# Performance work log

Hardware: AMD Instinct MI355X
Metric: run time of the kernel (lower is better)

The kernel has to match this reference:

```python
import jax, jax.numpy as jnp
import numpy as np

B, T, D, L, E = 4096, 4, 1024, 2, 4  # batch, tasks (risk_num+1), dim, layers, experts/task


def setup_inputs() -> dict:
    key = jax.random.key(0)
    ks = jax.random.split(key, 9)
    s = 1.0 / np.sqrt(D).astype(np.float32)  # torch Linear-style uniform scale
    se = 1.0 / np.sqrt(E).astype(np.float32)
    u = lambda k, shape, sc: jax.random.uniform(k, shape, jnp.float32, -sc, sc)
    return {
        "x": jax.random.normal(ks[0], (B, T, D), jnp.float32),
        # per-layer, per-task shared-expert MLP params (mlp_level=2)
        "W1": u(ks[1], (L, T, D, D), s), "b1": u(ks[2], (L, T, D), s),
        "W2": u(ks[3], (L, T, D, D), s), "b2": u(ks[4], (L, T, D), s),
        # integration weights over E (aliased) experts per task
        "inte": u(ks[5], (L, T, E), se),
        # one shared gate per layer: Linear(D -> T) + softmax
        "Wg": u(ks[6], (L, D, T), s), "bg": u(ks[7], (L, T), s),
    }


def reference(x, W1, b1, W2, b2, inte, Wg, bg):
    h = x  # [B, T, D]
    n_layers = W1.shape[0]
    for l in range(n_layers):
        # per-task 2-layer MLP expert (all E experts per task share weights in the
        # original due to [MLP]*E aliasing)
        t1 = jax.nn.relu(jnp.einsum('btd,tdo->bto', h, W1[l]) + b1[l])
        t2 = jax.nn.relu(jnp.einsum('btd,tdo->bto', t1, W2[l]) + b2[l])
        # stack of E identical expert outputs einsum'd with inte weights == scale by sum_e w[t,e]
        teo = t2 * jnp.sum(inte[l], axis=-1)[None, :, None]  # [B, T, D]
        # shared gate applied to each task's output: softmax(Linear(teo)) -> [B, T, T]
        g = jax.nn.softmax(jnp.einsum('btd,dk->btk', teo, Wg[l]) + bg[l], axis=-1)
        # bmm combine + residual
        h = jnp.einsum('btk,bkd->btd', g, teo) + teo
    return h
```

## Files before the change

kernel.cpp:

```cpp
#include <hip/hip_runtime.h>
#include <hip/hip_bf16.h>

#define B_ 4096
#define T_ 4
#define D_ 1024
#define E_ 4

typedef unsigned short ushort_t;
typedef float f32x4 __attribute__((ext_vector_type(4)));
typedef short bf16x8 __attribute__((ext_vector_type(8)));

__device__ __forceinline__ unsigned short f2bf(float f) {
    unsigned int u = __float_as_uint(f);
    u += 0x7FFF + ((u >> 16) & 1);
    return (unsigned short)(u >> 16);
}

#define GLOBAL_LOAD_LDS16(gp, lp)                                                        \
    __builtin_amdgcn_global_load_lds((const __attribute__((address_space(1))) void*)(gp),\
                                     (__attribute__((address_space(3))) void*)(lp),      \
                                     16, 0, 0)

__global__ __launch_bounds__(256) void k_convert_x(const float* __restrict__ x,
                                                   ushort_t* __restrict__ hbf) {
    int idx = (blockIdx.x * 256 + threadIdx.x) * 4;
    int d = idx & (D_ - 1);
    int t = (idx >> 10) & 3;
    int b = idx >> 12;
    const float4 v = *(const float4*)(x + idx);
    ushort4 o = { f2bf(v.x), f2bf(v.y), f2bf(v.z), f2bf(v.w) };
    *(ushort4*)(hbf + (size_t)t * B_ * D_ + (size_t)b * D_ + d) = o;
}

__global__ __launch_bounds__(256) void k_transpose_w(const float* __restrict__ W1,
                                                     const float* __restrict__ W2,
                                                     ushort_t* __restrict__ W1t,
                                                     ushort_t* __restrict__ W2t) {
    __shared__ float tile[32][33];
    const int z = blockIdx.z;
    const float* src = (z < 8) ? (W1 + (size_t)z * D_ * D_) : (W2 + (size_t)(z - 8) * D_ * D_);
    ushort_t* dst = (z < 8) ? (W1t + (size_t)z * D_ * D_) : (W2t + (size_t)(z - 8) * D_ * D_);
    const int o0 = blockIdx.x * 32, d0 = blockIdx.y * 32;
    const int tx = threadIdx.x, ty = threadIdx.y;
#pragma unroll
    for (int j = 0; j < 4; ++j)
        tile[ty + 8 * j][tx] = src[(size_t)(d0 + ty + 8 * j) * D_ + o0 + tx];
    __syncthreads();
#pragma unroll
    for (int j = 0; j < 4; ++j)
        dst[(size_t)(o0 + ty + 8 * j) * D_ + d0 + tx] = f2bf(tile[tx][ty + 8 * j]);
}

template <bool OUT_BF16>
__global__ __launch_bounds__(512, 4) void k_gemm_bt(
    const ushort_t* __restrict__ A,
    const ushort_t* __restrict__ Bt,
    const float* __restrict__ bias,
    void* __restrict__ out,
    const float* __restrict__ inte)
{
    const int f = blockIdx.x;
    const int xcd = f & 7;
    const int t = xcd >> 1;
    const int m_blk = ((f >> 6) << 1) | (xcd & 1);
    const int n_blk = (f >> 3) & 7;
    const int m0 = m_blk * 256, n0 = n_blk * 128;

    const ushort_t* Ap = A + (size_t)t * B_ * D_;
    const ushort_t* Bp = Bt + (size_t)t * D_ * D_;
    const float* bp = bias + t * D_;

    __shared__ __align__(16) ushort_t As[2][256 * 32];
    __shared__ __align__(16) ushort_t Bs[2][128 * 32];

    const int tid = threadIdx.x;
    const int lane = tid & 63, wid = tid >> 6;
    const int lr = lane & 15, quad = lane >> 4;
    const int wm = (wid & 3) * 64, wn = (wid >> 2) * 64;

    f32x4 acc[4][4] = {};

    const int qa0 = wid * 64 + lane;
    const int qa1 = qa0 + 512;
    const int qb  = qa0;
    const ushort_t* ga0 = Ap + (size_t)(m0 + (qa0 >> 2)) * D_ + (qa0 & 3) * 8;
    const ushort_t* ga1 = Ap + (size_t)(m0 + (qa1 >> 2)) * D_ + (qa1 & 3) * 8;
    const ushort_t* gb  = Bp + (size_t)(n0 + (qb  >> 2)) * D_ + (qb  & 3) * 8;

#define STAGE(k0, s)                                              \
    do {                                                          \
        GLOBAL_LOAD_LDS16(ga0 + (k0), As[s] + wid * 512);         \
        GLOBAL_LOAD_LDS16(ga1 + (k0), As[s] + 4096 + wid * 512);  \
        GLOBAL_LOAD_LDS16(gb  + (k0), Bs[s] + wid * 512);         \
    } while (0)

    STAGE(0, 0);
    int s = 0;
    for (int k0 = 0; k0 < D_; k0 += 32, s ^= 1) {
        __syncthreads();
        if (k0 + 32 < D_) STAGE(k0 + 32, s ^ 1);
        bf16x8 af[4], bfv[4];
#pragma unroll
        for (int mi = 0; mi < 4; ++mi)
            af[mi] = *(const bf16x8*)(As[s] + (wm + mi * 16 + lr) * 32 + quad * 8);
#pragma unroll
        for (int ni = 0; ni < 4; ++ni)
            bfv[ni] = *(const bf16x8*)(Bs[s] + (wn + ni * 16 + lr) * 32 + quad * 8);
#pragma unroll
        for (int mi = 0; mi < 4; ++mi)
#pragma unroll
            for (int ni = 0; ni < 4; ++ni)
                acc[mi][ni] = __builtin_amdgcn_mfma_f32_16x16x32_bf16(
                    af[mi], bfv[ni], acc[mi][ni], 0, 0, 0);
    }
#undef STAGE

    float scale = 1.0f;
    if (inte) {
        const float* ip = inte + t * E_;
        scale = ip[0] + ip[1] + ip[2] + ip[3];
    }
#pragma unroll
    for (int mi = 0; mi < 4; ++mi) {
#pragma unroll
        for (int ni = 0; ni < 4; ++ni) {
            const int gcol = n0 + wn + ni * 16 + lr;
            const float bv = bp[gcol];
#pragma unroll
            for (int r = 0; r < 4; ++r) {
                const int grow = m0 + wm + mi * 16 + quad * 4 + r;
                float v = acc[mi][ni][r] + bv;
                v = fmaxf(v, 0.0f) * scale;
                const size_t off = (size_t)t * B_ * D_ + (size_t)grow * D_ + gcol;
                if (OUT_BF16) ((ushort_t*)out)[off] = f2bf(v);
                else          ((float*)out)[off] = v;
            }
        }
    }
}

template <bool FINAL>
__global__ __launch_bounds__(256) void k_gate_combine(
    const float* __restrict__ teo,
    const float* __restrict__ Wg,
    const float* __restrict__ bg,
    void* __restrict__ out)
{
    const int b = blockIdx.x;
    const int tid = threadIdx.x;
    const int d0 = tid * 4;

    float4 tv[4];
#pragma unroll
    for (int t = 0; t < 4; ++t)
        tv[t] = *(const float4*)(teo + (size_t)t * B_ * D_ + (size_t)b * D_ + d0);
    float4 wg[4];
#pragma unroll
    for (int i = 0; i < 4; ++i)
        wg[i] = *(const float4*)(Wg + (size_t)(d0 + i) * 4);

    float p[16];
#pragma unroll
    for (int t = 0; t < 4; ++t) {
        const float* tvp = (const float*)&tv[t];
#pragma unroll
        for (int k = 0; k < 4; ++k) {
            p[t * 4 + k] = tvp[0] * ((const float*)&wg[0])[k]
                         + tvp[1] * ((const float*)&wg[1])[k]
                         + tvp[2] * ((const float*)&wg[2])[k]
                         + tvp[3] * ((const float*)&wg[3])[k];
        }
    }
#pragma unroll
    for (int i = 0; i < 16; ++i) {
        float v = p[i];
        v += __shfl_xor(v, 1, 64);
        v += __shfl_xor(v, 2, 64);
        v += __shfl_xor(v, 4, 64);
        v += __shfl_xor(v, 8, 64);
        p[i] = v;
    }
    __shared__ float red[16][16];
    __shared__ float fin[16];
    const int grp = tid >> 4;
    if ((tid & 15) == 0) {
#pragma unroll
        for (int i = 0; i < 16; ++i) red[grp][i] = p[i];
    }
    __syncthreads();
    if (tid < 16) {
        float v = 0.0f;
#pragma unroll
        for (int g = 0; g < 16; ++g) v += red[g][tid];
        fin[tid] = v;
    }
    __syncthreads();

    float g[4][4];
#pragma unroll
    for (int t = 0; t < 4; ++t) {
        float lg[4];
#pragma unroll
        for (int k = 0; k < 4; ++k)
            lg[k] = fin[t * 4 + k] + bg[k];
        float mx = fmaxf(fmaxf(lg[0], lg[1]), fmaxf(lg[2], lg[3]));
        float e0 = __expf(lg[0] - mx), e1 = __expf(lg[1] - mx);
        float e2 = __expf(lg[2] - mx), e3 = __expf(lg[3] - mx);
        float inv = 1.0f / (e0 + e1 + e2 + e3);
        g[t][0] = e0 * inv; g[t][1] = e1 * inv; g[t][2] = e2 * inv; g[t][3] = e3 * inv;
    }
#pragma unroll
    for (int t = 0; t < 4; ++t) {
        float o[4];
#pragma unroll
        for (int i = 0; i < 4; ++i) {
            o[i] = g[t][0] * ((const float*)&tv[0])[i]
                 + g[t][1] * ((const float*)&tv[1])[i]
                 + g[t][2] * ((const float*)&tv[2])[i]
                 + g[t][3] * ((const float*)&tv[3])[i]
                 + ((const float*)&tv[t])[i];
        }
        if (FINAL) {
            float4 ov = { o[0], o[1], o[2], o[3] };
            *(float4*)((float*)out + (size_t)b * T_ * D_ + (size_t)t * D_ + d0) = ov;
        } else {
            ushort4 ov = { f2bf(o[0]), f2bf(o[1]), f2bf(o[2]), f2bf(o[3]) };
            *(ushort4*)((ushort_t*)out + (size_t)t * B_ * D_ + (size_t)b * D_ + d0) = ov;
        }
    }
}

extern "C" void kernel_launch(void* const* d_in, const int* in_sizes, int n_in,
                              void* d_out, int out_size, void* d_ws, size_t ws_size,
                              hipStream_t stream) {
    const float* x    = (const float*)d_in[0];
    const float* W1   = (const float*)d_in[1];
    const float* b1   = (const float*)d_in[2];
    const float* W2   = (const float*)d_in[3];
    const float* b2   = (const float*)d_in[4];
    const float* inte = (const float*)d_in[5];
    const float* Wg   = (const float*)d_in[6];
    const float* bg   = (const float*)d_in[7];

    char* ws = (char*)d_ws;
    ushort_t* W1t  = (ushort_t*)(ws);
    ushort_t* W2t  = (ushort_t*)(ws + 33554432);
    ushort_t* Hbf  = (ushort_t*)(ws + 67108864);
    ushort_t* T1bf = (ushort_t*)(ws + 100663296);
    float*    Teo  = (float*)   (ws + 134217728);

    k_convert_x<<<dim3(B_ * T_ * D_ / 1024), 256, 0, stream>>>(x, Hbf);
    k_transpose_w<<<dim3(D_ / 32, D_ / 32, 16), dim3(32, 8), 0, stream>>>(W1, W2, W1t, W2t);

    for (int l = 0; l < 2; ++l) {
        const size_t wOff = (size_t)l * T_ * D_ * D_;
        k_gemm_bt<true ><<<dim3(512), 512, 0, stream>>>(Hbf, W1t + wOff, b1 + l * T_ * D_,
                                                        (void*)T1bf, nullptr);
        k_gemm_bt<false><<<dim3(512), 512, 0, stream>>>(T1bf, W2t + wOff, b2 + l * T_ * D_,
                                                        (void*)Teo, inte + l * T_ * E_);
        if (l == 0)
            k_gate_combine<false><<<dim3(B_), 256, 0, stream>>>(
                Teo, Wg + l * D_ * T_, bg + l * T_, (void*)Hbf);
        else
            k_gate_combine<true ><<<dim3(B_), 256, 0, stream>>>(
                Teo, Wg + l * D_ * T_, bg + l * T_, (void*)d_out);
    }
}
```

Measured before the change: 377.9 us.

## Use 32x32 MFMA with swizzled LDS, merge prep kernels, bf16 layer-0 teo

```diff
diff --git a/kernel.cpp b/kernel.cpp
--- a/kernel.cpp
+++ b/kernel.cpp
@@ -7,7 +7,7 @@
 #define E_ 4
 
 typedef unsigned short ushort_t;
-typedef float f32x4 __attribute__((ext_vector_type(4)));
+typedef float f32x16 __attribute__((ext_vector_type(16)));
 typedef short bf16x8 __attribute__((ext_vector_type(8)));
 
 __device__ __forceinline__ unsigned short f2bf(float f) {
@@ -15,33 +15,42 @@
     u += 0x7FFF + ((u >> 16) & 1);
     return (unsigned short)(u >> 16);
 }
+__device__ __forceinline__ float bf2f(unsigned short u) {
+    return __uint_as_float(((unsigned int)u) << 16);
+}
 
 #define GLOBAL_LOAD_LDS16(gp, lp)                                                        \
     __builtin_amdgcn_global_load_lds((const __attribute__((address_space(1))) void*)(gp),\
                                      (__attribute__((address_space(3))) void*)(lp),      \
                                      16, 0, 0)
 
-__global__ __launch_bounds__(256) void k_convert_x(const float* __restrict__ x,
-                                                   ushort_t* __restrict__ hbf) {
-    int idx = (blockIdx.x * 256 + threadIdx.x) * 4;
-    int d = idx & (D_ - 1);
-    int t = (idx >> 10) & 3;
-    int b = idx >> 12;
-    const float4 v = *(const float4*)(x + idx);
-    ushort4 o = { f2bf(v.x), f2bf(v.y), f2bf(v.z), f2bf(v.w) };
-    *(ushort4*)(hbf + (size_t)t * B_ * D_ + (size_t)b * D_ + d) = o;
-}
-
-__global__ __launch_bounds__(256) void k_transpose_w(const float* __restrict__ W1,
-                                                     const float* __restrict__ W2,
-                                                     ushort_t* __restrict__ W1t,
-                                                     ushort_t* __restrict__ W2t) {
+#define LSLOT_E(row, kq) (((((row) << 2) + ((kq) ^ (((row) >> 1) & 3)))) << 3)
+#define KQOF(q) ((((q) & 3) ^ (((q) >> 3) & 3)) * 8)
+
+__global__ __launch_bounds__(256) void k_prep(const float* __restrict__ x,
+                                              const float* __restrict__ W1,
+                                              const float* __restrict__ W2,
+                                              ushort_t* __restrict__ hbf,
+                                              ushort_t* __restrict__ W1t,
+                                              ushort_t* __restrict__ W2t) {
+    const int z = blockIdx.z;
+    const int tid = threadIdx.x;
+    if (z >= 16) {
+        const int blk = (z - 16) * 1024 + blockIdx.y * 32 + blockIdx.x;
+        const int idx = (blk * 256 + tid) * 4;
+        const int d = idx & (D_ - 1);
+        const int t = (idx >> 10) & 3;
+        const int b = idx >> 12;
+        const float4 v = *(const float4*)(x + idx);
+        ushort4 o = { f2bf(v.x), f2bf(v.y), f2bf(v.z), f2bf(v.w) };
+        *(ushort4*)(hbf + (size_t)t * B_ * D_ + (size_t)b * D_ + d) = o;
+        return;
+    }
     __shared__ float tile[32][33];
-    const int z = blockIdx.z;
     const float* src = (z < 8) ? (W1 + (size_t)z * D_ * D_) : (W2 + (size_t)(z - 8) * D_ * D_);
     ushort_t* dst = (z < 8) ? (W1t + (size_t)z * D_ * D_) : (W2t + (size_t)(z - 8) * D_ * D_);
     const int o0 = blockIdx.x * 32, d0 = blockIdx.y * 32;
-    const int tx = threadIdx.x, ty = threadIdx.y;
+    const int tx = tid & 31, ty = tid >> 5;
 #pragma unroll
     for (int j = 0; j < 4; ++j)
         tile[ty + 8 * j][tx] = src[(size_t)(d0 + ty + 8 * j) * D_ + o0 + tx];
@@ -75,17 +84,17 @@
 
     const int tid = threadIdx.x;
     const int lane = tid & 63, wid = tid >> 6;
-    const int lr = lane & 15, quad = lane >> 4;
+    const int l31 = lane & 31, lh = lane >> 5;
     const int wm = (wid & 3) * 64, wn = (wid >> 2) * 64;
 
-    f32x4 acc[4][4] = {};
+    f32x16 acc[2][2] = {};
 
     const int qa0 = wid * 64 + lane;
     const int qa1 = qa0 + 512;
     const int qb  = qa0;
-    const ushort_t* ga0 = Ap + (size_t)(m0 + (qa0 >> 2)) * D_ + (qa0 & 3) * 8;
-    const ushort_t* ga1 = Ap + (size_t)(m0 + (qa1 >> 2)) * D_ + (qa1 & 3) * 8;
-    const ushort_t* gb  = Bp + (size_t)(n0 + (qb  >> 2)) * D_ + (qb  & 3) * 8;
+    const ushort_t* ga0 = Ap + (size_t)(m0 + (qa0 >> 2)) * D_ + KQOF(qa0);
+    const ushort_t* ga1 = Ap + (size_t)(m0 + (qa1 >> 2)) * D_ + KQOF(qa1);
+    const ushort_t* gb  = Bp + (size_t)(n0 + (qb  >> 2)) * D_ + KQOF(qb);
 
 #define STAGE(k0, s)                                              \
     do {                                                          \
@@ -99,19 +108,25 @@
     for (int k0 = 0; k0 < D_; k0 += 32, s ^= 1) {
         __syncthreads();
         if (k0 + 32 < D_) STAGE(k0 + 32, s ^ 1);
-        bf16x8 af[4], bfv[4];
-#pragma unroll
-        for (int mi = 0; mi < 4; ++mi)
-            af[mi] = *(const bf16x8*)(As[s] + (wm + mi * 16 + lr) * 32 + quad * 8);
-#pragma unroll
-        for (int ni = 0; ni < 4; ++ni)
-            bfv[ni] = *(const bf16x8*)(Bs[s] + (wn + ni * 16 + lr) * 32 + quad * 8);
-#pragma unroll
-        for (int mi = 0; mi < 4; ++mi)
-#pragma unroll
-            for (int ni = 0; ni < 4; ++ni)
-                acc[mi][ni] = __builtin_amdgcn_mfma_f32_16x16x32_bf16(
-                    af[mi], bfv[ni], acc[mi][ni], 0, 0, 0);
+        bf16x8 af[2][2], bfv[2][2];
+#pragma unroll
+        for (int mi = 0; mi < 2; ++mi)
+#pragma unroll
+            for (int ks = 0; ks < 2; ++ks)
+                af[mi][ks] = *(const bf16x8*)(As[s] + LSLOT_E(wm + mi * 32 + l31, ks * 2 + lh));
+#pragma unroll
+        for (int ni = 0; ni < 2; ++ni)
+#pragma unroll
+            for (int ks = 0; ks < 2; ++ks)
+                bfv[ni][ks] = *(const bf16x8*)(Bs[s] + LSLOT_E(wn + ni * 32 + l31, ks * 2 + lh));
+#pragma unroll
+        for (int ks = 0; ks < 2; ++ks)
+#pragma unroll
+            for (int mi = 0; mi < 2; ++mi)
+#pragma unroll
+                for (int ni = 0; ni < 2; ++ni)
+                    acc[mi][ni] = __builtin_amdgcn_mfma_f32_32x32x16_bf16(
+                        af[mi][ks], bfv[ni][ks], acc[mi][ni], 0, 0, 0);
     }
 #undef STAGE
 
@@ -121,15 +136,15 @@
         scale = ip[0] + ip[1] + ip[2] + ip[3];
     }
 #pragma unroll
-    for (int mi = 0; mi < 4; ++mi) {
-#pragma unroll
-        for (int ni = 0; ni < 4; ++ni) {
-            const int gcol = n0 + wn + ni * 16 + lr;
+    for (int mi = 0; mi < 2; ++mi) {
+#pragma unroll
+        for (int ni = 0; ni < 2; ++ni) {
+            const int gcol = n0 + wn + ni * 32 + l31;
             const float bv = bp[gcol];
 #pragma unroll
-            for (int r = 0; r < 4; ++r) {
-                const int grow = m0 + wm + mi * 16 + quad * 4 + r;
-                float v = acc[mi][ni][r] + bv;
+            for (int reg = 0; reg < 16; ++reg) {
+                const int grow = m0 + wm + mi * 32 + (reg & 3) + 8 * (reg >> 2) + 4 * lh;
+                float v = acc[mi][ni][reg] + bv;
                 v = fmaxf(v, 0.0f) * scale;
                 const size_t off = (size_t)t * B_ * D_ + (size_t)grow * D_ + gcol;
                 if (OUT_BF16) ((ushort_t*)out)[off] = f2bf(v);
@@ -139,9 +154,9 @@
     }
 }
 
-template <bool FINAL>
+template <bool FINAL, bool TEO_BF16>
 __global__ __launch_bounds__(256) void k_gate_combine(
-    const float* __restrict__ teo,
+    const void* __restrict__ teo_v,
     const float* __restrict__ Wg,
     const float* __restrict__ bg,
     void* __restrict__ out)
@@ -152,8 +167,16 @@
 
     float4 tv[4];
 #pragma unroll
-    for (int t = 0; t < 4; ++t)
-        tv[t] = *(const float4*)(teo + (size_t)t * B_ * D_ + (size_t)b * D_ + d0);
+    for (int t = 0; t < 4; ++t) {
+        if (TEO_BF16) {
+            const ushort4 u = *(const ushort4*)((const ushort_t*)teo_v +
+                                 (size_t)t * B_ * D_ + (size_t)b * D_ + d0);
+            tv[t] = { bf2f(u.x), bf2f(u.y), bf2f(u.z), bf2f(u.w) };
+        } else {
+            tv[t] = *(const float4*)((const float*)teo_v +
+                                 (size_t)t * B_ * D_ + (size_t)b * D_ + d0);
+        }
+    }
     float4 wg[4];
 #pragma unroll
     for (int i = 0; i < 4; ++i)
@@ -247,22 +270,24 @@
     ushort_t* W2t  = (ushort_t*)(ws + 33554432);
     ushort_t* Hbf  = (ushort_t*)(ws + 67108864);
     ushort_t* T1bf = (ushort_t*)(ws + 100663296);
-    float*    Teo  = (float*)   (ws + 134217728);
-
-    k_convert_x<<<dim3(B_ * T_ * D_ / 1024), 256, 0, stream>>>(x, Hbf);
-    k_transpose_w<<<dim3(D_ / 32, D_ / 32, 16), dim3(32, 8), 0, stream>>>(W1, W2, W1t, W2t);
+    void*     Teo  = (void*)    (ws + 134217728);
+
+    k_prep<<<dim3(32, 32, 32), 256, 0, stream>>>(x, W1, W2, Hbf, W1t, W2t);
 
     for (int l = 0; l < 2; ++l) {
         const size_t wOff = (size_t)l * T_ * D_ * D_;
-        k_gemm_bt<true ><<<dim3(512), 512, 0, stream>>>(Hbf, W1t + wOff, b1 + l * T_ * D_,
-                                                        (void*)T1bf, nullptr);
-        k_gemm_bt<false><<<dim3(512), 512, 0, stream>>>(T1bf, W2t + wOff, b2 + l * T_ * D_,
-                                                        (void*)Teo, inte + l * T_ * E_);
-        if (l == 0)
-            k_gate_combine<false><<<dim3(B_), 256, 0, stream>>>(
+        k_gemm_bt<true><<<dim3(512), 512, 0, stream>>>(Hbf, W1t + wOff, b1 + l * T_ * D_,
+                                                       (void*)T1bf, nullptr);
+        if (l == 0) {
+            k_gemm_bt<true ><<<dim3(512), 512, 0, stream>>>(T1bf, W2t + wOff, b2 + l * T_ * D_,
+                                                            Teo, inte + l * T_ * E_);
+            k_gate_combine<false, true ><<<dim3(B_), 256, 0, stream>>>(
                 Teo, Wg + l * D_ * T_, bg + l * T_, (void*)Hbf);
-        else
-            k_gate_combine<true ><<<dim3(B_), 256, 0, stream>>>(
+        } else {
+            k_gemm_bt<false><<<dim3(512), 512, 0, stream>>>(T1bf, W2t + wOff, b2 + l * T_ * D_,
+                                                            Teo, inte + l * T_ * E_);
+            k_gate_combine<true , false><<<dim3(B_), 256, 0, stream>>>(
                 Teo, Wg + l * D_ * T_, bg + l * T_, (void*)d_out);
-    }
-}
+        }
+    }
+}
```

Result: slower. 389.0 us (+2.9%).
